# Optimization experiments

Hardware: AMD Instinct MI355X
Metric: run time of the kernel (lower is better)

The kernel has to match this reference:

```python
import jax, jax.numpy as jnp
import numpy as np
from jax import lax

D_MODEL = 1024
D_STATE = 128
HEADDIM = 64
EXPAND = 2
NGROUPS = 1
CHUNK = 256
D_INNER = EXPAND * D_MODEL          # 2048
D_SSM = D_INNER                      # d_ssm defaults to d_inner
NHEADS = D_SSM // HEADDIM            # 32
CONV_DIM = D_SSM + 2 * NGROUPS * D_STATE   # 2304
D_IN_PROJ = 2 * D_INNER + 2 * NGROUPS * D_STATE + NHEADS  # 4384 -> d_mlp = 0
BATCH = 2
SEQLEN = 2048
EPS = 1e-5


def setup_inputs() -> dict:
    key = jax.random.key(0)
    ks = jax.random.split(key, 9)
    u = jax.random.normal(ks[0], (BATCH, SEQLEN, D_MODEL), jnp.float32)
    # indices into left-padded (len = SEQLEN+1) sequence; 0 selects the zero pad
    conv_indices = jax.random.randint(ks[1], (BATCH, 4 * SEQLEN), 0, SEQLEN + 1)
    W_in = jax.random.normal(ks[2], (D_IN_PROJ, D_MODEL), jnp.float32) / np.sqrt(D_MODEL).astype(np.float32)
    conv_w = jax.random.normal(ks[3], (CONV_DIM, 4), jnp.float32) * 0.2
    conv_b = jax.random.normal(ks[4], (CONV_DIM,), jnp.float32) * 0.02
    # dt_bias init exactly as the module: inverse-softplus of dt in [dt_min, dt_max]
    dt = jnp.exp(jax.random.uniform(ks[5], (NHEADS,), jnp.float32) * (np.log(0.1) - np.log(0.001)) + np.log(0.001))
    dt = jnp.clip(dt, 1e-4)
    dt_bias = dt + jnp.log(-jnp.expm1(-dt))
    A_log = jnp.log(jax.random.uniform(ks[6], (NHEADS,), jnp.float32, minval=1.0, maxval=16.0))
    D = jnp.ones((NHEADS,), jnp.float32)
    norm_w = jnp.ones((D_SSM,), jnp.float32)
    W_out = jax.random.normal(ks[7], (D_MODEL, D_INNER), jnp.float32) / np.sqrt(D_INNER).astype(np.float32)
    return dict(u=u, conv_indices=conv_indices, W_in=W_in, conv_w=conv_w, conv_b=conv_b,
                dt_bias=dt_bias, A_log=A_log, D=D, norm_w=norm_w, W_out=W_out)


def _segsum(x):
    # x: (b, c, h, cs) -> (b, c, h, cs, cs); out[..., t, s] = sum_{k=s+1..t} x[..., k]
    cs = x.shape[-1]
    cx = jnp.cumsum(x, axis=-1)
    diff = cx[..., :, None] - cx[..., None, :]
    mask = jnp.tril(jnp.ones((cs, cs), dtype=bool))
    return jnp.where(mask, diff, -jnp.inf)


def _ssd(x, dt, A, Bh, Ch, D):
    # Mamba2 SSD chunked scan. x:(b,l,h,p), dt:(b,l,h), A:(h,), Bh/Ch:(b,l,h,n), D:(h,)
    b, l, h, p = x.shape
    n = Bh.shape[-1]
    c = l // CHUNK
    xr = x.reshape(b, c, CHUNK, h, p)
    dtr = dt.reshape(b, c, CHUNK, h)
    Br = Bh.reshape(b, c, CHUNK, h, n)
    Cr = Ch.reshape(b, c, CHUNK, h, n)
    dA = dtr * A                                 # (b,c,cs,h)
    Acum = jnp.cumsum(dA, axis=2)                # (b,c,cs,h)
    Lm = jnp.exp(_segsum(jnp.transpose(dA, (0, 1, 3, 2))))  # (b,c,h,cs,cs)
    dtx = xr * dtr[..., None]                    # dt-weighted inputs
    # intra-chunk (diagonal blocks)
    Yd = jnp.einsum('bcthn,bcshn,bchts,bcshp->bcthp', Cr, Br, Lm, dtx)
    # per-chunk final states
    decay_states = jnp.exp(Acum[:, :, -1:, :] - Acum)        # (b,c,cs,h)
    states = jnp.einsum('bcshn,bcsh,bcshp->bchpn', Br, decay_states, dtx)
    chunk_decay = jnp.exp(Acum[:, :, -1, :])     # (b,c,h)
    def step(h_prev, inp):
        dec, st = inp
        return h_prev * dec[..., None, None] + st, h_prev
    init = jnp.zeros((b, h, p, n), x.dtype)
    _, prev = lax.scan(step, init, (jnp.moveaxis(chunk_decay, 1, 0), jnp.moveaxis(states, 1, 0)))
    prev = jnp.moveaxis(prev, 0, 1)              # (b,c,h,p,n): state entering each chunk
    # inter-chunk (off-diagonal) contribution
    Yoff = jnp.einsum('bcthn,bchpn,bcth->bcthp', Cr, prev, jnp.exp(Acum))
    Y = Yd + Yoff + D[None, None, None, :, None] * xr
    return Y.reshape(b, l, h, p)


def reference(u, conv_indices, W_in, conv_w, conv_b, dt_bias, A_log, D, norm_w, W_out):
    b, l, _ = u.shape
    zxbcdt = u @ W_in.T                          # (b,l,4384); d_mlp == 0
    z, xBC, dt_raw = jnp.split(zxbcdt, [D_SSM, D_SSM + CONV_DIM], axis=-1)
    # tree conv: left-pad seq by 1, gather 4 tree positions per output step, depthwise conv k=4 stride=4
    xc = jnp.transpose(xBC, (0, 2, 1))           # (b, conv_dim, l)
    xp = jnp.pad(xc, ((0, 0), (0, 0), (1, 0)))
    idx = jnp.broadcast_to(conv_indices[:, None, :], (b, CONV_DIM, 4 * l))
    g = jnp.take_along_axis(xp, idx, axis=2).reshape(b, CONV_DIM, l, 4)
    conv = jnp.einsum('bclk,ck->bcl', g, conv_w) + conv_b[None, :, None]
    xBC = jax.nn.silu(jnp.transpose(conv, (0, 2, 1)))  # (b,l,conv_dim)
    x, Bm, Cm = jnp.split(xBC, [D_SSM, D_SSM + NGROUPS * D_STATE], axis=-1)
    x = x.reshape(b, l, NHEADS, HEADDIM)
    hpg = NHEADS // NGROUPS
    Bh = jnp.repeat(Bm.reshape(b, l, NGROUPS, D_STATE), hpg, axis=2)
    Ch = jnp.repeat(Cm.reshape(b, l, NGROUPS, D_STATE), hpg, axis=2)
    dt = jax.nn.softplus(dt_raw + dt_bias)       # dt_softplus=True, default dt_limit
    A = -jnp.exp(A_log.astype(jnp.float32))
    y = _ssd(x, dt, A, Bh, Ch, D).reshape(b, l, D_SSM)
    # RMSNormGated, norm_before_gate=False, group_size = d_ssm (ngroups=1)
    yz = y * jax.nn.silu(z)
    var = jnp.mean(jnp.square(yz), axis=-1, keepdims=True)
    y = yz * lax.rsqrt(var + EPS) * norm_w
    return y @ W_out.T
```

## Files before the change

### kernel.cpp

```cpp
#include <hip/hip_runtime.h>

#define BB 2
#define LL 2048
#define DMODEL 1024
#define DSSM 2048
#define NH 32
#define HD 64
#define DST 128
#define CONVD 2304
#define DPROJ 4384
#define CS 64
#define NC 32
#define BLTOT (BB*LL)

typedef short v8s __attribute__((ext_vector_type(8)));
typedef float v4f __attribute__((ext_vector_type(4)));

__device__ __forceinline__ float b2f(unsigned short h) {
  union { unsigned int u; float f; } v; v.u = ((unsigned int)h) << 16; return v.f;
}
__device__ __forceinline__ unsigned short f2b(float f) {
  union { float f; unsigned int u; } v; v.f = f;
  unsigned int u = v.u;
  return (unsigned short)((u + 0x7fffu + ((u >> 16) & 1u)) >> 16);
}
__device__ __forceinline__ v4f mfma16(v8s a, v8s b, v4f c) {
  return __builtin_amdgcn_mfma_f32_16x16x32_bf16(a, b, c, 0, 0, 0);
}
__device__ __forceinline__ void gl_lds16(const unsigned short* g, unsigned short* l) {
  __builtin_amdgcn_global_load_lds(
      (const __attribute__((address_space(1))) void*)(g),
      (__attribute__((address_space(3))) void*)(l), 16, 0, 0);
}

__global__ __launch_bounds__(256) void cvt3_kernel(
    const float* __restrict__ a, unsigned short* __restrict__ oa, int na4,
    const float* __restrict__ b, unsigned short* __restrict__ ob, int nb4,
    const float* __restrict__ c, unsigned short* __restrict__ oc, int nc4)
{
  int i = blockIdx.x * 256 + threadIdx.x;
  const float* src; unsigned short* dst; int j;
  if (i < na4) { src = a; dst = oa; j = i; }
  else if (i < na4 + nb4) { src = b; dst = ob; j = i - na4; }
  else if (i < na4 + nb4 + nc4) { src = c; dst = oc; j = i - na4 - nb4; }
  else return;
  float4 v = ((const float4*)src)[j];
  ushort4 o;
  o.x = f2b(v.x); o.y = f2b(v.y); o.z = f2b(v.z); o.w = f2b(v.w);
  ((ushort4*)dst)[j] = o;
}

template<int TN, int OUT_BF16>
__global__ __launch_bounds__(256) void gemm_bt(
    const unsigned short* __restrict__ A, const unsigned short* __restrict__ Bt,
    void* __restrict__ Cout, int M, int N, int K, int ldc)
{
  constexpr int NT = TN / 32;
  const int bm = blockIdx.x, bn = blockIdx.y;
  const int tid = threadIdx.x;
  const int wave = tid >> 6, lane = tid & 63;
  const int wm = wave & 1, wn = wave >> 1;
  const int q = lane >> 4, lr = lane & 15;

  __shared__ __align__(16) unsigned short As[128 * 64];
  __shared__ __align__(16) unsigned short Bs[TN * 64];

  v4f acc[4][NT];
#pragma unroll
  for (int i = 0; i < 4; i++)
#pragma unroll
    for (int j = 0; j < NT; j++) acc[i][j] = v4f{0.f, 0.f, 0.f, 0.f};

  const int lrow = lane >> 3;
  const int gchunk = (lane & 7) ^ lrow;

  for (int k0 = 0; k0 < K; k0 += 64) {
    __syncthreads();
#pragma unroll
    for (int it = 0; it < 4; ++it) {
      int r = wave * 32 + it * 8 + lrow;
      gl_lds16(A + (size_t)(bm * 128 + r) * K + k0 + gchunk * 8,
               &As[(wave * 32 + it * 8) * 64]);
    }
#pragma unroll
    for (int it = 0; it < TN / 32; ++it) {
      int rloc = wave * (TN / 4) + it * 8;
      int rb = bn * TN + rloc + lrow; if (rb >= N) rb = N - 1;
      gl_lds16(Bt + (size_t)rb * K + k0 + gchunk * 8, &Bs[rloc * 64]);
    }
    __syncthreads();
#pragma unroll
    for (int ks = 0; ks < 64; ks += 32) {
      const int c0 = (ks >> 3) + q;
      v8s af[4], bf[NT];
#pragma unroll
      for (int mt = 0; mt < 4; ++mt) {
        int r = wm * 64 + mt * 16 + lr;
        af[mt] = *(const v8s*)&As[r * 64 + ((c0 ^ (r & 7)) << 3)];
      }
#pragma unroll
      for (int nt = 0; nt < NT; ++nt) {
        int r = wn * (TN / 2) + nt * 16 + lr;
        bf[nt] = *(const v8s*)&Bs[r * 64 + ((c0 ^ (r & 7)) << 3)];
      }
#pragma unroll
      for (int mt = 0; mt < 4; ++mt)
#pragma unroll
        for (int nt = 0; nt < NT; ++nt)
          acc[mt][nt] = mfma16(af[mt], bf[nt], acc[mt][nt]);
    }
  }
#pragma unroll
  for (int mt = 0; mt < 4; ++mt) {
#pragma unroll
    for (int nt = 0; nt < NT; ++nt) {
      int row = bm * 128 + wm * 64 + mt * 16 + q * 4;
      int col = bn * TN + wn * (TN / 2) + nt * 16 + lr;
      if (col < N) {
#pragma unroll
        for (int r = 0; r < 4; ++r) {
          float v = acc[mt][nt][r];
          if (OUT_BF16) ((unsigned short*)Cout)[(size_t)(row + r) * ldc + col] = f2b(v);
          else          ((float*)Cout)[(size_t)(row + r) * ldc + col] = v;
        }
      }
    }
  }
}

__global__ __launch_bounds__(256) void conv_kernel(
    const unsigned short* __restrict__ C1, const int* __restrict__ cidx,
    const float* __restrict__ convw, const float* __restrict__ convb,
    const float* __restrict__ dtbias,
    unsigned short* __restrict__ x16, unsigned short* __restrict__ Bg16,
    unsigned short* __restrict__ Cg16, float* __restrict__ dtb)
{
  int bl0 = blockIdx.x * 4;
  int b = bl0 >> 11;
  int tid = threadIdx.x;
  __shared__ int idxs[16];
  if (tid < 16) {
    int tk = tid >> 2, k = tid & 3;
    idxs[tid] = cidx[b * (4 * LL) + (((bl0 + tk) & 2047) * 4) + k];
  }
  __syncthreads();
  const float4* cw4 = (const float4*)convw;
#pragma unroll
  for (int it = 0; it < 3; ++it) {
    int unit = tid + it * 256;
    if (unit >= CONVD / 4) break;
    int c4 = unit * 4;
    float4 w0 = cw4[c4], w1 = cw4[c4 + 1], w2 = cw4[c4 + 2], w3 = cw4[c4 + 3];
    float4 cb = *(const float4*)(convb + c4);
#pragma unroll
    for (int tk = 0; tk < 4; ++tk) {
      int bl = bl0 + tk;
      ushort4 rv[4];
#pragma unroll
      for (int k = 0; k < 4; ++k) {
        int iv = idxs[tk * 4 + k];
        rv[k] = (iv > 0) ? *(const ushort4*)(C1 + (size_t)(b * LL + iv - 1) * DPROJ + DSSM + c4)
                         : make_ushort4(0, 0, 0, 0);
      }
      float a0 = cb.x + b2f(rv[0].x) * w0.x + b2f(rv[1].x) * w0.y + b2f(rv[2].x) * w0.z + b2f(rv[3].x) * w0.w;
      float a1 = cb.y + b2f(rv[0].y) * w1.x + b2f(rv[1].y) * w1.y + b2f(rv[2].y) * w1.z + b2f(rv[3].y) * w1.w;
      float a2 = cb.z + b2f(rv[0].z) * w2.x + b2f(rv[1].z) * w2.y + b2f(rv[2].z) * w2.z + b2f(rv[3].z) * w2.w;
      float a3 = cb.w + b2f(rv[0].w) * w3.x + b2f(rv[1].w) * w3.y + b2f(rv[2].w) * w3.z + b2f(rv[3].w) * w3.w;
      ushort4 o;
      o.x = f2b(a0 / (1.f + __expf(-a0)));
      o.y = f2b(a1 / (1.f + __expf(-a1)));
      o.z = f2b(a2 / (1.f + __expf(-a2)));
      o.w = f2b(a3 / (1.f + __expf(-a3)));
      if (c4 < DSSM)            *(ushort4*)(x16 + (size_t)bl * DSSM + c4) = o;
      else if (c4 < DSSM + DST) *(ushort4*)(Bg16 + (size_t)bl * DST + (c4 - DSSM)) = o;
      else                      *(ushort4*)(Cg16 + (size_t)bl * DST + (c4 - DSSM - DST)) = o;
    }
  }
  if (tid < 4 * NH) {
    int tk = tid >> 5, hh = tid & 31;
    int bl = bl0 + tk;
    float raw = b2f(C1[(size_t)bl * DPROJ + DSSM + CONVD + hh]) + dtbias[hh];
    float dtv = (raw > 20.f) ? raw : log1pf(__expf(raw));
    dtb[(size_t)bl * NH + hh] = dtv;
  }
}

__global__ __launch_bounds__(256) void d1_intra(
    const unsigned short* __restrict__ x16, const unsigned short* __restrict__ Bg16,
    const unsigned short* __restrict__ Cg16, const float* __restrict__ dtb,
    const float* __restrict__ A_log, const float* __restrict__ Dp,
    unsigned short* __restrict__ y16, unsigned short* __restrict__ statesb,
    float* __restrict__ cdb, float* __restrict__ acumb)
{
  int gid = blockIdx.x;
  int h = gid & 31, ci = (gid >> 5) & 31, b = gid >> 10;
  int tid = threadIdx.x, wave = tid >> 6, lane = tid & 63, q = lane >> 4, lr = lane & 15;

  __shared__ __align__(16) unsigned short BnG[CS * 136];
  __shared__ __align__(16) unsigned short BTw[DST * 72];
  __shared__ __align__(16) unsigned short xT[HD * 72];
  __shared__ float dt_s[CS], ac_s[CS], dec_s[CS];

  const size_t blbase = (size_t)b * LL + ci * CS;
  const size_t chbase = (size_t)(b * NC + ci) * NH + h;
  float Ah = -__expf(A_log[h]);

  if (wave == 0) {
    float d = dtb[(blbase + lane) * NH + h];
    float a = d * Ah;
#pragma unroll
    for (int off = 1; off < 64; off <<= 1) {
      float u = __shfl_up(a, off, 64);
      if (lane >= off) a += u;
    }
    float tot = __shfl(a, 63, 64);
    dt_s[lane] = d;
    ac_s[lane] = a;
    dec_s[lane] = __expf(tot - a);
    acumb[chbase * CS + lane] = a;
    if (lane == 0) cdb[chbase] = __expf(tot);
  }

#pragma unroll
  for (int g = 0; g < 8; ++g) {
    int f = g * 256 + tid;
    int s = f >> 5, c4 = (f & 31) * 4;
    *(ushort4*)&BnG[s * 136 + c4] = *(const ushort4*)(Bg16 + (blbase + s) * DST + c4);
  }
#pragma unroll
  for (int g = 0; g < 4; ++g) {
    int f = g * 256 + tid;
    int s = f >> 4, p4 = (f & 15) * 4;
    ushort4 xv = *(const ushort4*)(x16 + (blbase + s) * DSSM + h * HD + p4);
    xT[(p4 + 0) * 72 + s] = xv.x;
    xT[(p4 + 1) * 72 + s] = xv.y;
    xT[(p4 + 2) * 72 + s] = xv.z;
    xT[(p4 + 3) * 72 + s] = xv.w;
  }
  __syncthreads();

#pragma unroll
  for (int g = 0; g < 4; ++g) {
    int f = g * 256 + tid;
    int n = f >> 3, sg = f & 7;
    int s0 = sg * 8;
    ushort4 lo, hi;
    lo.x = f2b(b2f(BnG[(s0 + 0) * 136 + n]) * dec_s[s0 + 0] * dt_s[s0 + 0]);
    lo.y = f2b(b2f(BnG[(s0 + 1) * 136 + n]) * dec_s[s0 + 1] * dt_s[s0 + 1]);
    lo.z = f2b(b2f(BnG[(s0 + 2) * 136 + n]) * dec_s[s0 + 2] * dt_s[s0 + 2]);
    lo.w = f2b(b2f(BnG[(s0 + 3) * 136 + n]) * dec_s[s0 + 3] * dt_s[s0 + 3]);
    hi.x = f2b(b2f(BnG[(s0 + 4) * 136 + n]) * dec_s[s0 + 4] * dt_s[s0 + 4]);
    hi.y = f2b(b2f(BnG[(s0 + 5) * 136 + n]) * dec_s[s0 + 5] * dt_s[s0 + 5]);
    hi.z = f2b(b2f(BnG[(s0 + 6) * 136 + n]) * dec_s[s0 + 6] * dt_s[s0 + 6]);
    hi.w = f2b(b2f(BnG[(s0 + 7) * 136 + n]) * dec_s[s0 + 7] * dt_s[s0 + 7]);
    *(ushort4*)&BTw[n * 72 + s0] = lo;
    *(ushort4*)&BTw[n * 72 + s0 + 4] = hi;
  }

  v4f accS[4];
#pragma unroll
  for (int i = 0; i < 4; i++) accS[i] = v4f{0.f, 0.f, 0.f, 0.f};
#pragma unroll
  for (int ks = 0; ks < 128; ks += 32) {
    v8s a = *(const v8s*)(Cg16 + (blbase + wave * 16 + lr) * DST + ks + q * 8);
#pragma unroll
    for (int si = 0; si < 4; ++si) {
      v8s bb = *(const v8s*)&BnG[(si * 16 + lr) * 136 + ks + q * 8];
      accS[si] = mfma16(a, bb, accS[si]);
    }
  }
  __syncthreads();

  {
    int tbase = wave * 16 + q * 4;
#pragma unroll
    for (int si = 0; si < 4; ++si) {
      int s = si * 16 + lr;
      float ds = dt_s[s], as = ac_s[s];
#pragma unroll
      for (int r = 0; r < 4; ++r) {
        int tt = tbase + r;
        float g = 0.f;
        if (s <= tt) g = accS[si][r] * __expf(ac_s[tt] - as) * ds;
        BnG[tt * 72 + s] = f2b(g);
      }
    }
  }
  __syncthreads();

  v4f accY[4], accPT[4][2];
#pragma unroll
  for (int i = 0; i < 4; i++) {
    accY[i] = v4f{0.f,0.f,0.f,0.f};
    accPT[i][0] = v4f{0.f,0.f,0.f,0.f};
    accPT[i][1] = v4f{0.f,0.f,0.f,0.f};
  }
  int nw = wave * 32;
#pragma unroll
  for (int ks = 0; ks < 64; ks += 32) {
    v8s xf[4];
#pragma unroll
    for (int i = 0; i < 4; ++i) xf[i] = *(const v8s*)&xT[(i * 16 + lr) * 72 + ks + q * 8];
    v8s aG  = *(const v8s*)&BnG[(wave * 16 + lr) * 72 + ks + q * 8];
    v8s bw0 = *(const v8s*)&BTw[(nw + lr) * 72 + ks + q * 8];
    v8s bw1 = *(const v8s*)&BTw[(nw + 16 + lr) * 72 + ks + q * 8];
#pragma unroll
    for (int nt = 0; nt < 4; ++nt) {
      accY[nt] = mfma16(aG, xf[nt], accY[nt]);
      accPT[nt][0] = mfma16(xf[nt], bw0, accPT[nt][0]);
      accPT[nt][1] = mfma16(xf[nt], bw1, accPT[nt][1]);
    }
  }

  float Dh = Dp[h];
#pragma unroll
  for (int nt = 0; nt < 4; ++nt) {
    int p = nt * 16 + lr;
#pragma unroll
    for (int r = 0; r < 4; ++r) {
      int t = wave * 16 + q * 4 + r;
      float xv = b2f(xT[p * 72 + t]);
      y16[(blbase + t) * DSSM + h * HD + p] = f2b(accY[nt][r] + Dh * xv);
    }
  }
  size_t sbase = chbase * (DST * HD);
#pragma unroll
  for (int mt = 0; mt < 4; ++mt) {
#pragma unroll
    for (int nt = 0; nt < 2; ++nt) {
      int n = nw + nt * 16 + lr;
#pragma unroll
      for (int r = 0; r < 4; ++r) {
        int p = mt * 16 + q * 4 + r;
        statesb[sbase + (size_t)p * DST + n] = f2b(accPT[mt][nt][r]);
      }
    }
  }
}

__global__ __launch_bounds__(256) void d2_scan(
    unsigned short* __restrict__ statesb, const float* __restrict__ cdb)
{
  int g = blockIdx.x;
  int seg = g & 31, bh = g >> 5;
  int b = bh >> 5, h = bh & 31;
  int e = seg * 256 + threadIdx.x;
  const size_t cstride = (size_t)NH * DST * HD;
  size_t base = ((size_t)(b * NC) * NH + h) * (DST * HD) + e;
  unsigned short st[NC];
#pragma unroll
  for (int ci = 0; ci < NC; ++ci) st[ci] = statesb[base + ci * cstride];
  float run = 0.f;
#pragma unroll
  for (int ci = 0; ci < NC; ++ci) {
    float cd = cdb[(b * NC + ci) * NH + h];
    statesb[base + ci * cstride] = f2b(run);
    run = run * cd + b2f(st[ci]);
  }
}

__global__ __launch_bounds__(256) void d3_inter(
    const unsigned short* __restrict__ Cg16,
    const unsigned short* __restrict__ statesb, const float* __restrict__ acumb,
    unsigned short* __restrict__ y16)
{
  int gid = blockIdx.x;
  int h = gid & 31, ci = (gid >> 5) & 31, b = gid >> 10;
  int tid = threadIdx.x, wave = tid >> 6, lane = tid & 63, q = lane >> 4, lr = lane & 15;
  __shared__ __align__(16) unsigned short pT[HD * 136];
  __shared__ __align__(16) float ys[CS * 68];
  __shared__ float ea[CS];
  const size_t blbase = (size_t)b * LL + ci * CS;
  const size_t chbase = (size_t)(b * NC + ci) * NH + h;
  if (tid < CS) ea[tid] = __expf(acumb[chbase * CS + tid]);
  size_t sbase = chbase * (DST * HD);
#pragma unroll
  for (int g = 0; g < 8; ++g) {
    int f = g * 256 + tid;
    int p = f >> 5, c4 = (f & 31) * 4;
    *(ushort4*)&pT[p * 136 + c4] = *(const ushort4*)(statesb + sbase + (size_t)p * DST + c4);
  }
  __syncthreads();
  v4f acc[4];
#pragma unroll
  for (int i = 0; i < 4; i++) acc[i] = v4f{0.f, 0.f, 0.f, 0.f};
#pragma unroll
  for (int ks = 0; ks < 128; ks += 32) {
    v8s a = *(const v8s*)(Cg16 + (blbase + wave * 16 + lr) * DST + ks + q * 8);
#pragma unroll
    for (int nt = 0; nt < 4; ++nt) {
      v8s bb = *(const v8s*)&pT[(nt * 16 + lr) * 136 + ks + q * 8];
      acc[nt] = mfma16(a, bb, acc[nt]);
    }
  }
#pragma unroll
  for (int nt = 0; nt < 4; ++nt) {
#pragma unroll
    for (int r = 0; r < 4; ++r)
      ys[(wave * 16 + q * 4 + r) * 68 + nt * 16 + lr] = acc[nt][r];
  }
  __syncthreads();
#pragma unroll
  for (int it = 0; it < 2; ++it) {
    int unit = it * 256 + tid;
    int t = unit >> 3, p8 = (unit & 7) * 8;
    float ea_t = ea[t];
    size_t off = (blbase + t) * DSSM + h * HD + p8;
    uint4 yv = *(const uint4*)(y16 + off);
    float4 o0 = *(const float4*)&ys[t * 68 + p8];
    float4 o1 = *(const float4*)&ys[t * 68 + p8 + 4];
    const unsigned int* yu = (const unsigned int*)&yv;
    float oo[8] = {o0.x, o0.y, o0.z, o0.w, o1.x, o1.y, o1.z, o1.w};
    unsigned int ro[4];
#pragma unroll
    for (int d = 0; d < 4; ++d) {
      unsigned short y0 = (unsigned short)(yu[d] & 0xffffu), y1 = (unsigned short)(yu[d] >> 16);
      float v0 = b2f(y0) + ea_t * oo[d * 2 + 0];
      float v1 = b2f(y1) + ea_t * oo[d * 2 + 1];
      ro[d] = (unsigned int)f2b(v0) | ((unsigned int)f2b(v1) << 16);
    }
    *(uint4*)(y16 + off) = make_uint4(ro[0], ro[1], ro[2], ro[3]);
  }
}

__global__ __launch_bounds__(256) void norm_kernel(
    const unsigned short* __restrict__ y16, const unsigned short* __restrict__ C1,
    const float* __restrict__ normw, unsigned short* __restrict__ yzn)
{
  int bl = blockIdx.x;
  int tid = threadIdx.x;
  int wave = tid >> 6, lane = tid & 63;
  int c8 = tid * 8;
  uint4 yv = *(const uint4*)(y16 + (size_t)bl * DSSM + c8);
  uint4 zv = *(const uint4*)(C1 + (size_t)bl * DPROJ + c8);
  const unsigned int* yu = (const unsigned int*)&yv;
  const unsigned int* zu = (const unsigned int*)&zv;
  float vals[8];
  float ss = 0.f;
#pragma unroll
  for (int d = 0; d < 4; ++d) {
    unsigned short y0 = (unsigned short)(yu[d] & 0xffffu), y1 = (unsigned short)(yu[d] >> 16);
    unsigned short z0 = (unsigned short)(zu[d] & 0xffffu), z1 = (unsigned short)(zu[d] >> 16);
    float zf0 = b2f(z0), zf1 = b2f(z1);
    float v0 = b2f(y0) * (zf0 / (1.f + __expf(-zf0)));
    float v1 = b2f(y1) * (zf1 / (1.f + __expf(-zf1)));
    vals[d * 2] = v0; vals[d * 2 + 1] = v1;
    ss += v0 * v0 + v1 * v1;
  }
#pragma unroll
  for (int off = 32; off > 0; off >>= 1) ss += __shfl_down(ss, off);
  __shared__ float red[4];
  if (lane == 0) red[wave] = ss;
  __syncthreads();
  float tot = red[0] + red[1] + red[2] + red[3];
  float scale = rsqrtf(tot * (1.f / 2048.f) + 1e-5f);
  float4 w0 = *(const float4*)(normw + c8);
  float4 w1 = *(const float4*)(normw + c8 + 4);
  float ws[8] = {w0.x, w0.y, w0.z, w0.w, w1.x, w1.y, w1.z, w1.w};
  unsigned int ro[4];
#pragma unroll
  for (int d = 0; d < 4; ++d) {
    unsigned short r0 = f2b(vals[d * 2] * scale * ws[d * 2]);
    unsigned short r1 = f2b(vals[d * 2 + 1] * scale * ws[d * 2 + 1]);
    ro[d] = (unsigned int)r0 | ((unsigned int)r1 << 16);
  }
  *(uint4*)(yzn + (size_t)bl * DSSM + c8) = make_uint4(ro[0], ro[1], ro[2], ro[3]);
}

extern "C" void kernel_launch(void* const* d_in, const int* in_sizes, int n_in,
                              void* d_out, int out_size, void* d_ws, size_t ws_size,
                              hipStream_t stream) {
  const float* u      = (const float*)d_in[0];
  const int*   cidx   = (const int*)d_in[1];
  const float* W_in   = (const float*)d_in[2];
  const float* convw  = (const float*)d_in[3];
  const float* convb  = (const float*)d_in[4];
  const float* dtbias = (const float*)d_in[5];
  const float* A_log  = (const float*)d_in[6];
  const float* Dp     = (const float*)d_in[7];
  const float* normw  = (const float*)d_in[8];
  const float* W_out  = (const float*)d_in[9];

  char* w = (char*)d_ws;
  size_t off = 0;
  auto alloc = [&](size_t bytes) { char* p = w + off; off += (bytes + 255) & ~(size_t)255; return p; };
  unsigned short* u16     = (unsigned short*)alloc((size_t)BLTOT * DMODEL * 2);
  unsigned short* Win16   = (unsigned short*)alloc((size_t)DPROJ * DMODEL * 2);
  unsigned short* Wout16  = (unsigned short*)alloc((size_t)DMODEL * DSSM * 2);
  unsigned short* C1      = (unsigned short*)alloc((size_t)BLTOT * DPROJ * 2);
  unsigned short* x16     = (unsigned short*)alloc((size_t)BLTOT * DSSM * 2);
  unsigned short* Bg16    = (unsigned short*)alloc((size_t)BLTOT * DST * 2);
  unsigned short* Cg16    = (unsigned short*)alloc((size_t)BLTOT * DST * 2);
  float*          dtb     = (float*)alloc((size_t)BLTOT * NH * 4);
  float*          acumb   = (float*)alloc((size_t)BB * NC * NH * CS * 4);
  unsigned short* y16     = (unsigned short*)alloc((size_t)BLTOT * DSSM * 2);
  unsigned short* statesb = (unsigned short*)alloc((size_t)BB * NC * NH * DST * HD * 2);
  float*          cdb     = (float*)alloc((size_t)BB * NC * NH * 4);
  unsigned short* yzn     = (unsigned short*)alloc((size_t)BLTOT * DSSM * 2);

  const int na4 = BLTOT * DMODEL / 4, nb4 = DPROJ * DMODEL / 4, nc4 = DMODEL * DSSM / 4;
  cvt3_kernel<<<(na4 + nb4 + nc4 + 255) / 256, 256, 0, stream>>>(
      u, u16, na4, W_in, Win16, nb4, W_out, Wout16, nc4);

  gemm_bt<128, 1><<<dim3(BLTOT / 128, (DPROJ + 127) / 128), 256, 0, stream>>>(
      u16, Win16, C1, BLTOT, DPROJ, DMODEL, DPROJ);
  conv_kernel<<<BLTOT / 4, 256, 0, stream>>>(C1, cidx, convw, convb, dtbias, x16, Bg16, Cg16, dtb);
  d1_intra<<<BB * NC * NH, 256, 0, stream>>>(x16, Bg16, Cg16, dtb, A_log, Dp, y16, statesb, cdb, acumb);
  d2_scan<<<BB * NH * 32, 256, 0, stream>>>(statesb, cdb);
  d3_inter<<<BB * NC * NH, 256, 0, stream>>>(Cg16, statesb, acumb, y16);
  norm_kernel<<<BLTOT, 256, 0, stream>>>(y16, C1, normw, yzn);
  gemm_bt<64, 0><<<dim3(BLTOT / 128, DMODEL / 64), 256, 0, stream>>>(
      yzn, Wout16, (float*)d_out, BLTOT, DMODEL, DSSM, DMODEL);
}
```

Baseline: 260.8 us.

## Fuse inter-chunk state scan into inter-chunk output kernel

```diff
diff --git a/kernel.cpp b/kernel.cpp
--- a/kernel.cpp
+++ b/kernel.cpp
@@ -338,88 +338,80 @@
   }
 }
 
-__global__ __launch_bounds__(256) void d2_scan(
-    unsigned short* __restrict__ statesb, const float* __restrict__ cdb)
-{
-  int g = blockIdx.x;
-  int seg = g & 31, bh = g >> 5;
-  int b = bh >> 5, h = bh & 31;
-  int e = seg * 256 + threadIdx.x;
-  const size_t cstride = (size_t)NH * DST * HD;
-  size_t base = ((size_t)(b * NC) * NH + h) * (DST * HD) + e;
-  unsigned short st[NC];
-#pragma unroll
-  for (int ci = 0; ci < NC; ++ci) st[ci] = statesb[base + ci * cstride];
-  float run = 0.f;
-#pragma unroll
-  for (int ci = 0; ci < NC; ++ci) {
-    float cd = cdb[(b * NC + ci) * NH + h];
-    statesb[base + ci * cstride] = f2b(run);
-    run = run * cd + b2f(st[ci]);
-  }
-}
-
-__global__ __launch_bounds__(256) void d3_inter(
+__global__ __launch_bounds__(256) void d23_kernel(
     const unsigned short* __restrict__ Cg16,
-    const unsigned short* __restrict__ statesb, const float* __restrict__ acumb,
+    const unsigned short* __restrict__ statesb,
+    const float* __restrict__ acumb, const float* __restrict__ cdb,
     unsigned short* __restrict__ y16)
 {
   int gid = blockIdx.x;
-  int h = gid & 31, ci = (gid >> 5) & 31, b = gid >> 10;
+  int pq = gid & 3, h = (gid >> 2) & 31, b = gid >> 7;
+  int p0 = pq * 16;
   int tid = threadIdx.x, wave = tid >> 6, lane = tid & 63, q = lane >> 4, lr = lane & 15;
-  __shared__ __align__(16) unsigned short pT[HD * 136];
-  __shared__ __align__(16) float ys[CS * 68];
-  __shared__ float ea[CS];
-  const size_t blbase = (size_t)b * LL + ci * CS;
-  const size_t chbase = (size_t)(b * NC + ci) * NH + h;
-  if (tid < CS) ea[tid] = __expf(acumb[chbase * CS + tid]);
-  size_t sbase = chbase * (DST * HD);
-#pragma unroll
-  for (int g = 0; g < 8; ++g) {
-    int f = g * 256 + tid;
-    int p = f >> 5, c4 = (f & 31) * 4;
-    *(ushort4*)&pT[p * 136 + c4] = *(const ushort4*)(statesb + sbase + (size_t)p * DST + c4);
-  }
-  __syncthreads();
-  v4f acc[4];
-#pragma unroll
-  for (int i = 0; i < 4; i++) acc[i] = v4f{0.f, 0.f, 0.f, 0.f};
-#pragma unroll
-  for (int ks = 0; ks < 128; ks += 32) {
-    v8s a = *(const v8s*)(Cg16 + (blbase + wave * 16 + lr) * DST + ks + q * 8);
-#pragma unroll
-    for (int nt = 0; nt < 4; ++nt) {
-      v8s bb = *(const v8s*)&pT[(nt * 16 + lr) * 136 + ks + q * 8];
-      acc[nt] = mfma16(a, bb, acc[nt]);
-    }
-  }
-#pragma unroll
-  for (int nt = 0; nt < 4; ++nt) {
+
+  __shared__ __align__(16) unsigned short S[2][16 * 136];
+  __shared__ float ea[2][CS];
+  __shared__ __align__(16) float ys[CS * 20];
+
+  int sp = tid >> 4, sn = (tid & 15) * 8;
+  float run[8];
+#pragma unroll
+  for (int j = 0; j < 8; ++j) run[j] = 0.f;
+
+  const unsigned short* sa0 =
+      statesb + ((size_t)(b * NC + 0) * NH + h) * (DST * HD) + (size_t)(p0 + sp) * DST + sn;
+  ushort4 stA = *(const ushort4*)(sa0);
+  ushort4 stB = *(const ushort4*)(sa0 + 4);
+
+  for (int ci = 0; ci < NC; ++ci) {
+    int buf = ci & 1;
+    const size_t blbase = (size_t)b * LL + ci * CS;
+    const size_t chbase = (size_t)(b * NC + ci) * NH + h;
+    {
+      unsigned short* sd = &S[buf][sp * 136 + sn];
+      ushort4 o0, o1;
+      o0.x = f2b(run[0]); o0.y = f2b(run[1]); o0.z = f2b(run[2]); o0.w = f2b(run[3]);
+      o1.x = f2b(run[4]); o1.y = f2b(run[5]); o1.z = f2b(run[6]); o1.w = f2b(run[7]);
+      *(ushort4*)sd = o0; *(ushort4*)(sd + 4) = o1;
+    }
+    if (tid < CS) ea[buf][tid] = __expf(acumb[chbase * CS + tid]);
+    __syncthreads();
+    int cn = (ci + 1 < NC) ? ci + 1 : ci;
+    const unsigned short* san =
+        statesb + ((size_t)(b * NC + cn) * NH + h) * (DST * HD) + (size_t)(p0 + sp) * DST + sn;
+    ushort4 nstA = *(const ushort4*)(san);
+    ushort4 nstB = *(const ushort4*)(san + 4);
+    v4f acc = v4f{0.f, 0.f, 0.f, 0.f};
+#pragma unroll
+    for (int ks = 0; ks < 128; ks += 32) {
+      v8s a = *(const v8s*)(Cg16 + (blbase + wave * 16 + lr) * DST + ks + q * 8);
+      v8s bb = *(const v8s*)&S[buf][lr * 136 + ks + q * 8];
+      acc = mfma16(a, bb, acc);
+    }
 #pragma unroll
     for (int r = 0; r < 4; ++r)
-      ys[(wave * 16 + q * 4 + r) * 68 + nt * 16 + lr] = acc[nt][r];
-  }
-  __syncthreads();
-#pragma unroll
-  for (int it = 0; it < 2; ++it) {
-    int unit = it * 256 + tid;
-    int t = unit >> 3, p8 = (unit & 7) * 8;
-    float ea_t = ea[t];
-    size_t off = (blbase + t) * DSSM + h * HD + p8;
-    uint4 yv = *(const uint4*)(y16 + off);
-    float4 o0 = *(const float4*)&ys[t * 68 + p8];
-    float4 o1 = *(const float4*)&ys[t * 68 + p8 + 4];
-    const unsigned int* yu = (const unsigned int*)&yv;
-    float oo[8] = {o0.x, o0.y, o0.z, o0.w, o1.x, o1.y, o1.z, o1.w};
-    unsigned int ro[4];
-#pragma unroll
-    for (int d = 0; d < 4; ++d) {
-      unsigned short y0 = (unsigned short)(yu[d] & 0xffffu), y1 = (unsigned short)(yu[d] >> 16);
-      float v0 = b2f(y0) + ea_t * oo[d * 2 + 0];
-      float v1 = b2f(y1) + ea_t * oo[d * 2 + 1];
-      ro[d] = (unsigned int)f2b(v0) | ((unsigned int)f2b(v1) << 16);
-    }
-    *(uint4*)(y16 + off) = make_uint4(ro[0], ro[1], ro[2], ro[3]);
+      ys[(wave * 16 + q * 4 + r) * 20 + lr] = acc[r];
+    __syncthreads();
+    {
+      int t = tid >> 2, seg = tid & 3;
+      float ea_t = ea[buf][t];
+      size_t off = (blbase + t) * DSSM + h * HD + p0 + seg * 4;
+      uint2 yv = *(const uint2*)(y16 + off);
+      float o0 = ys[t * 20 + seg * 4 + 0], o1 = ys[t * 20 + seg * 4 + 1];
+      float o2 = ys[t * 20 + seg * 4 + 2], o3 = ys[t * 20 + seg * 4 + 3];
+      unsigned short y0 = (unsigned short)(yv.x & 0xffffu), y1 = (unsigned short)(yv.x >> 16);
+      unsigned short y2 = (unsigned short)(yv.y & 0xffffu), y3 = (unsigned short)(yv.y >> 16);
+      uint2 ro;
+      ro.x = (unsigned)f2b(b2f(y0) + ea_t * o0) | ((unsigned)f2b(b2f(y1) + ea_t * o1) << 16);
+      ro.y = (unsigned)f2b(b2f(y2) + ea_t * o2) | ((unsigned)f2b(b2f(y3) + ea_t * o3) << 16);
+      *(uint2*)(y16 + off) = ro;
+    }
+    float cd = cdb[chbase];
+    run[0] = run[0] * cd + b2f(stA.x); run[1] = run[1] * cd + b2f(stA.y);
+    run[2] = run[2] * cd + b2f(stA.z); run[3] = run[3] * cd + b2f(stA.w);
+    run[4] = run[4] * cd + b2f(stB.x); run[5] = run[5] * cd + b2f(stB.y);
+    run[6] = run[6] * cd + b2f(stB.z); run[7] = run[7] * cd + b2f(stB.w);
+    stA = nstA; stB = nstB;
   }
 }
 
@@ -506,8 +498,7 @@
       u16, Win16, C1, BLTOT, DPROJ, DMODEL, DPROJ);
   conv_kernel<<<BLTOT / 4, 256, 0, stream>>>(C1, cidx, convw, convb, dtbias, x16, Bg16, Cg16, dtb);
   d1_intra<<<BB * NC * NH, 256, 0, stream>>>(x16, Bg16, Cg16, dtb, A_log, Dp, y16, statesb, cdb, acumb);
-  d2_scan<<<BB * NH * 32, 256, 0, stream>>>(statesb, cdb);
-  d3_inter<<<BB * NC * NH, 256, 0, stream>>>(Cg16, statesb, acumb, y16);
+  d23_kernel<<<BB * NH * 4, 256, 0, stream>>>(Cg16, statesb, acumb, cdb, y16);
   norm_kernel<<<BLTOT, 256, 0, stream>>>(y16, C1, normw, yzn);
   gemm_bt<64, 0><<<dim3(BLTOT / 128, DMODEL / 64), 256, 0, stream>>>(
       yzn, Wout16, (float*)d_out, BLTOT, DMODEL, DSSM, DMODEL);
```

After: 298.1 us. 1.14x slower.
